# Kernel optimization log

Measured on AMD Instinct MI355X. Metric: run time of the kernel, lower is better.

Reference implementation:

```python
import jax, jax.numpy as jnp
import numpy as np

N_NODES = 40000      # batch of group nodes
DEGREE = 32          # neighbors (members) per node
NUM_USERS = 100000
NUM_GROUPS = 50000
EMBED_DIM = 64


def setup_inputs() -> dict:
    key = jax.random.key(0)
    ks = jax.random.split(key, 8)
    E = N_NODES * DEGREE
    d = EMBED_DIM
    return {
        "nodes": jax.random.randint(ks[0], (N_NODES,), 0, NUM_GROUPS),
        "neigh_idx": jax.random.randint(ks[1], (E,), 0, NUM_USERS),
        # edge i belongs to node segment_ids[i]; sorted, DEGREE edges per node
        "segment_ids": jnp.repeat(jnp.arange(N_NODES), DEGREE),
        "u2e_weight": jax.random.normal(ks[2], (NUM_USERS, d), jnp.float32) * 0.02,
        "g2e_weight": jax.random.normal(ks[3], (NUM_GROUPS, d), jnp.float32) * 0.02,
        "att1_w": jax.random.normal(ks[4], (d, 2 * d), jnp.float32) * (1.0 / np.sqrt(2 * d)),
        "att1_b": jnp.zeros((d,), jnp.float32),
        "att2_w": jax.random.normal(ks[5], (d, d), jnp.float32) * (1.0 / np.sqrt(d)),
        "att2_b": jnp.zeros((d,), jnp.float32),
        "att3_w": jax.random.normal(ks[6], (1, d), jnp.float32) * (1.0 / np.sqrt(d)),
        "att3_b": jnp.zeros((1,), jnp.float32),
    }


def _segment_softmax(logits, seg, num_segments):
    # numerically stable softmax within each node's neighbor segment
    m = jax.ops.segment_max(logits, seg, num_segments=num_segments)
    a = jnp.exp(logits - m[seg])
    s = jax.ops.segment_sum(a, seg, num_segments=num_segments)
    return a / s[seg]


def reference(nodes, neigh_idx, segment_ids, u2e_weight, g2e_weight,
              att1_w, att1_b, att2_w, att2_b, att3_w, att3_b):
    e_u = u2e_weight[neigh_idx]                 # [E, d] member embeddings
    g_rep = g2e_weight[nodes][segment_ids]      # [E, d] group query broadcast per edge
    x = jnp.concatenate([e_u, g_rep], axis=-1)  # [E, 2d]
    h = jax.nn.relu(x @ att1_w.T + att1_b)      # [E, d] (dropout inactive at eval)
    h = jax.nn.relu(h @ att2_w.T + att2_b)      # [E, d]
    logits = (h @ att3_w.T + att3_b)[:, 0]      # [E]
    att = _segment_softmax(logits, segment_ids, N_NODES)  # [E]
    # attention-weighted aggregation of member embeddings per node
    return jax.ops.segment_sum(att[:, None] * e_u, segment_ids, num_segments=N_NODES)  # [N, d]
```

## Files before the change

kernel.cpp:

```cpp
#include <hip/hip_runtime.h>
#include <hip/hip_bf16.h>

typedef __attribute__((ext_vector_type(8))) short short8;
typedef __attribute__((ext_vector_type(4))) float floatx4;

#define NNODES 40000
#define NPW 4
#define WAVES 8
#define NPB (NPW * WAVES)
#define NBLK (NNODES / NPB)

#define U2E_ELEMS (100000 * 64)
#define WS_ALIGN 256
#define WS_NEEDED ((size_t)U2E_ELEMS * 2 + WS_ALIGN)


__device__ __forceinline__ float bf2f(unsigned short s) {
    return __uint_as_float(((unsigned int)s) << 16);
}
__device__ __forceinline__ unsigned short f2bf(float f) {
    unsigned int u = __float_as_uint(f);
    u += 0x7fffu + ((u >> 16) & 1u);
    return (unsigned short)(u >> 16);
}
__device__ __forceinline__ unsigned short f2bf_fast(float f) {
#if __has_builtin(__builtin_amdgcn_cvt_pk_bf16_f32)
    auto r = __builtin_amdgcn_cvt_pk_bf16_f32(f, f);
    unsigned int u; __builtin_memcpy(&u, &r, 4);
    return (unsigned short)u;
#else
    return f2bf(f);
#endif
}
__device__ __forceinline__ short8 cvt8(const float* fp) {
    floatx4 a = *(const floatx4*)fp;
    floatx4 b = *(const floatx4*)(fp + 4);
    short8 r;
    #pragma unroll
    for (int j = 0; j < 4; ++j) {
        r[j]     = (short)f2bf_fast(a[j]);
        r[4 + j] = (short)f2bf_fast(b[j]);
    }
    return r;
}

__global__ __launch_bounds__(256) void convert_u2e(
    const float* __restrict__ u2e, unsigned short* __restrict__ ub) {
    const size_t i = ((size_t)blockIdx.x * 256 + threadIdx.x) * 8;
    if (i < U2E_ELEMS) *(short8*)(ub + i) = cvt8(u2e + i);
}

template<int PRE>
__global__ __launch_bounds__(512, 4) void gat_fused(
    const int*   __restrict__ nodes,
    const int*   __restrict__ neigh,
    const float* __restrict__ u2f,
    const unsigned short* __restrict__ u2b,
    const float* __restrict__ g2e,
    const float* __restrict__ w1,
    const float* __restrict__ b1,
    const float* __restrict__ w2,
    const float* __restrict__ b2,
    const float* __restrict__ w3,
    float* __restrict__ out)
{
    __shared__ alignas(16) short w1f[16 * 64 * 8];
    __shared__ alignas(16) short w2f[8 * 64 * 8];
    __shared__ alignas(16) short hbuf[WAVES][32 * 72];

    const int tid  = threadIdx.x;
    const int wv   = tid >> 6;
    const int lane = tid & 63;
    const int q    = lane >> 4;
    const int n16  = lane & 15;

    for (int i = tid; i < 16 * 64; i += 512) {
        int s = i >> 6, slot = i & 63;
        int nt = s >> 2, kc = s & 3;
        int row = nt * 16 + (slot & 15);
        int k   = kc * 32 + (slot >> 4) * 8;
        *(short8*)&w1f[i * 8] = cvt8(w1 + (size_t)row * 128 + k);
    }
    for (int i = tid; i < 8 * 64; i += 512) {
        int s = i >> 6, slot = i & 63;
        int nt = s >> 1, kc = s & 1;
        int row = nt * 16 + (slot & 15);
        int k   = kc * 32 + (slot >> 4) * 8;
        *(short8*)&w2f[i * 8] = cvt8(w2 + (size_t)row * 64 + k);
    }
    float b1v[4], b2v[4], w3v[4];
    #pragma unroll
    for (int nt = 0; nt < 4; ++nt) {
        b1v[nt] = b1[nt * 16 + n16];
        b2v[nt] = b2[nt * 16 + n16];
        w3v[nt] = w3[nt * 16 + n16];
    }
    __syncthreads();

    const int n0 = blockIdx.x * NPB + wv * NPW;

    int gc, vc, c0, c1;
    int gn, vn, d0, d1;
    short8 A00, A01, A10, A11, G0, G1;

    auto loadA = [&](int idx, int half) -> short8 {
        if (PRE) return *(const short8*)(u2b + (size_t)idx * 64 + half * 32 + q * 8);
        else     return cvt8(u2f + (size_t)idx * 64 + half * 32 + q * 8);
    };

    {
        gc = nodes[n0];
        size_t eb = (size_t)n0 * 32;
        vc = neigh[eb + (lane & 31)];
        c0 = neigh[eb + n16];
        c1 = neigh[eb + 16 + n16];
        A00 = loadA(c0, 0); A01 = loadA(c0, 1);
        A10 = loadA(c1, 0); A11 = loadA(c1, 1);
        G0  = cvt8(g2e + (size_t)gc * 64 + q * 8);
        G1  = cvt8(g2e + (size_t)gc * 64 + 32 + q * 8);
        int n1 = n0 + 1;
        gn = nodes[n1];
        size_t eb1 = (size_t)n1 * 32;
        vn = neigh[eb1 + (lane & 31)];
        d0 = neigh[eb1 + n16];
        d1 = neigh[eb1 + 16 + n16];
    }

    const floatx4 zero4 = {0.f, 0.f, 0.f, 0.f};

    for (int it = 0; it < NPW; ++it) {
        const int n = n0 + it;
        const short8 a00 = A00, a01 = A01, a10 = A10, a11 = A11, g0 = G0, g1 = G1;
        const int idxv = vc;

        floatx4 acc[2][4];
        #pragma unroll
        for (int mt = 0; mt < 2; ++mt)
            #pragma unroll
            for (int nt = 0; nt < 4; ++nt) acc[mt][nt] = zero4;
        #pragma unroll
        for (int kc = 0; kc < 4; ++kc) {
            short8 x0 = (kc == 0) ? a00 : (kc == 1) ? a01 : (kc == 2) ? g0 : g1;
            short8 x1 = (kc == 0) ? a10 : (kc == 1) ? a11 : (kc == 2) ? g0 : g1;
            #pragma unroll
            for (int nt = 0; nt < 4; ++nt) {
                short8 b = *(const short8*)&w1f[((nt * 4 + kc) * 64 + lane) * 8];
                acc[0][nt] = __builtin_amdgcn_mfma_f32_16x16x32_bf16(x0, b, acc[0][nt], 0, 0, 0);
                acc[1][nt] = __builtin_amdgcn_mfma_f32_16x16x32_bf16(x1, b, acc[1][nt], 0, 0, 0);
            }
        }

        if (it < NPW - 1) {
            A00 = loadA(d0, 0); A01 = loadA(d0, 1);
            A10 = loadA(d1, 0); A11 = loadA(d1, 1);
            G0  = cvt8(g2e + (size_t)gn * 64 + q * 8);
            G1  = cvt8(g2e + (size_t)gn * 64 + 32 + q * 8);
            gc = gn; vc = vn; c0 = d0; c1 = d1;
            int nn = n0 + it + 2; if (nn > NNODES - 1) nn = NNODES - 1;
            gn = nodes[nn];
            size_t eb2 = (size_t)nn * 32;
            vn = neigh[eb2 + (lane & 31)];
            d0 = neigh[eb2 + n16];
            d1 = neigh[eb2 + 16 + n16];
        }

        __builtin_amdgcn_wave_barrier();
        #pragma unroll
        for (int mt = 0; mt < 2; ++mt)
            #pragma unroll
            for (int nt = 0; nt < 4; ++nt)
                #pragma unroll
                for (int r = 0; r < 4; ++r) {
                    float v = fmaxf(acc[mt][nt][r] + b1v[nt], 0.f);
                    hbuf[wv][(mt * 16 + q * 4 + r) * 72 + nt * 16 + n16] = (short)f2bf_fast(v);
                }
        __builtin_amdgcn_wave_barrier();

        short8 a2[2][2];
        #pragma unroll
        for (int mt = 0; mt < 2; ++mt)
            #pragma unroll
            for (int kc = 0; kc < 2; ++kc)
                a2[mt][kc] = *(const short8*)&hbuf[wv][(mt * 16 + n16) * 72 + kc * 32 + q * 8];

        floatx4 acc2[2][4];
        #pragma unroll
        for (int mt = 0; mt < 2; ++mt)
            #pragma unroll
            for (int nt = 0; nt < 4; ++nt) acc2[mt][nt] = zero4;
        #pragma unroll
        for (int kc = 0; kc < 2; ++kc)
            #pragma unroll
            for (int nt = 0; nt < 4; ++nt) {
                short8 b = *(const short8*)&w2f[((nt * 2 + kc) * 64 + lane) * 8];
                acc2[0][nt] = __builtin_amdgcn_mfma_f32_16x16x32_bf16(a2[0][kc], b, acc2[0][nt], 0, 0, 0);
                acc2[1][nt] = __builtin_amdgcn_mfma_f32_16x16x32_bf16(a2[1][kc], b, acc2[1][nt], 0, 0, 0);
            }

        float tt[2][4];
        #pragma unroll
        for (int mt = 0; mt < 2; ++mt)
            #pragma unroll
            for (int r = 0; r < 4; ++r) {
                float s = 0.f;
                #pragma unroll
                for (int nt = 0; nt < 4; ++nt)
                    s = fmaf(fmaxf(acc2[mt][nt][r] + b2v[nt], 0.f), w3v[nt], s);
                s += __shfl_xor(s, 1, 64);
                s += __shfl_xor(s, 2, 64);
                s += __shfl_xor(s, 4, 64);
                s += __shfl_xor(s, 8, 64);
                tt[mt][r] = s;
            }
        const int j = n16 & 7;
        float v0 = (j & 2) ? ((j & 1) ? tt[0][3] : tt[0][2]) : ((j & 1) ? tt[0][1] : tt[0][0]);
        float v1 = (j & 2) ? ((j & 1) ? tt[1][3] : tt[1][2]) : ((j & 1) ? tt[1][1] : tt[1][0]);
        float vm = (j & 4) ? v1 : v0;
        const int m = lane & 31;
        const int src = ((m & 12) << 2) | (((m >> 4) & 1) << 2) | (m & 3);
        const float lg = __shfl(vm, src, 64);

        float mx = lg;
        #pragma unroll
        for (int off = 1; off < 32; off <<= 1)
            mx = fmaxf(mx, __shfl_xor(mx, off, 64));
        const float ex = __expf(lg - mx);
        float sm = ex;
        #pragma unroll
        for (int off = 1; off < 32; off <<= 1)
            sm += __shfl_xor(sm, off, 64);
        const float attv = ex / sm;

        float acco = 0.f;
        #pragma unroll 16
        for (int e2 = 0; e2 < 32; ++e2) {
            int   sidx = __builtin_amdgcn_readlane(idxv, e2);
            float a    = __uint_as_float(__builtin_amdgcn_readlane(__float_as_uint(attv), e2));
            float ev   = PRE ? bf2f(u2b[(size_t)sidx * 64 + lane])
                             : u2f[(size_t)sidx * 64 + lane];
            acco = fmaf(a, ev, acco);
        }
        out[(size_t)n * 64 + lane] = acco;
    }
}

extern "C" void kernel_launch(void* const* d_in, const int* in_sizes, int n_in,
                              void* d_out, int out_size, void* d_ws, size_t ws_size,
                              hipStream_t stream) {
    const int*   nodes = (const int*)d_in[0];
    const int*   neigh = (const int*)d_in[1];
    const float* u2e = (const float*)d_in[3];
    const float* g2e = (const float*)d_in[4];
    const float* w1  = (const float*)d_in[5];
    const float* b1  = (const float*)d_in[6];
    const float* w2  = (const float*)d_in[7];
    const float* b2  = (const float*)d_in[8];
    const float* w3  = (const float*)d_in[9];
    float* out = (float*)d_out;

    if (ws_size >= WS_NEEDED) {
        unsigned short* ub = (unsigned short*)(((uintptr_t)d_ws + WS_ALIGN - 1) & ~(uintptr_t)(WS_ALIGN - 1));
        hipLaunchKernelGGL(convert_u2e, dim3((U2E_ELEMS / 8 + 255) / 256), dim3(256),
                           0, stream, u2e, ub);
        hipLaunchKernelGGL(gat_fused<1>, dim3(NBLK), dim3(512), 0, stream,
                           nodes, neigh, u2e, ub, g2e, w1, b1, w2, b2, w3, out);
    } else {
        hipLaunchKernelGGL(gat_fused<0>, dim3(NBLK), dim3(512), 0, stream,
                           nodes, neigh, u2e, (const unsigned short*)nullptr,
                           g2e, w1, b1, w2, b2, w3, out);
    }
}
```

Baseline: 173.7 us.

## Keep layer-1 output in registers and reuse staged embeddings from LDS for aggregation

The MFMA operands are swapped so each layer computes the transposed product, and the weight rows are permuted so the layer-1 accumulators can be packed straight into layer-2 B operands, removing the hbuf LDS round trip. The member embeddings already held in registers are written to a swizzled per-wave LDS buffer, and the final weighted sum reads them from there instead of gathering u2e rows from global memory a second time. Bias and w3 vectors move to LDS, and the logit reduction becomes two cross-lane shuffles. The trade is extra LDS stores, plus a permuted layout whose index arithmetic must line up exactly with the MFMA fragment layout.

```diff
diff --git a/kernel.cpp b/kernel.cpp
--- a/kernel.cpp
+++ b/kernel.cpp
@@ -3,6 +3,7 @@
 
 typedef __attribute__((ext_vector_type(8))) short short8;
 typedef __attribute__((ext_vector_type(4))) float floatx4;
+typedef __attribute__((ext_vector_type(4))) unsigned int uintx4;
 
 #define NNODES 40000
 #define NPW 4
@@ -23,24 +24,26 @@
     u += 0x7fffu + ((u >> 16) & 1u);
     return (unsigned short)(u >> 16);
 }
-__device__ __forceinline__ unsigned short f2bf_fast(float f) {
+__device__ __forceinline__ unsigned int pk2bf(float lo, float hi) {
 #if __has_builtin(__builtin_amdgcn_cvt_pk_bf16_f32)
-    auto r = __builtin_amdgcn_cvt_pk_bf16_f32(f, f);
+    auto r = __builtin_amdgcn_cvt_pk_bf16_f32(lo, hi);
     unsigned int u; __builtin_memcpy(&u, &r, 4);
-    return (unsigned short)u;
+    return u;
 #else
-    return f2bf(f);
+    return (unsigned int)f2bf(lo) | ((unsigned int)f2bf(hi) << 16);
 #endif
 }
 __device__ __forceinline__ short8 cvt8(const float* fp) {
     floatx4 a = *(const floatx4*)fp;
     floatx4 b = *(const floatx4*)(fp + 4);
-    short8 r;
-    #pragma unroll
-    for (int j = 0; j < 4; ++j) {
-        r[j]     = (short)f2bf_fast(a[j]);
-        r[4 + j] = (short)f2bf_fast(b[j]);
-    }
+    uintx4 u;
+    u[0] = pk2bf(a[0], a[1]); u[1] = pk2bf(a[2], a[3]);
+    u[2] = pk2bf(b[0], b[1]); u[3] = pk2bf(b[2], b[3]);
+    short8 r; __builtin_memcpy(&r, &u, 16);
+    return r;
+}
+__device__ __forceinline__ short8 u4s8(uintx4 u) {
+    short8 r; __builtin_memcpy(&r, &u, 16);
     return r;
 }
 
@@ -48,6 +51,10 @@
     const float* __restrict__ u2e, unsigned short* __restrict__ ub) {
     const size_t i = ((size_t)blockIdx.x * 256 + threadIdx.x) * 8;
     if (i < U2E_ELEMS) *(short8*)(ub + i) = cvt8(u2e + i);
+}
+
+__device__ __forceinline__ int sigma_row(int dt, int m) {
+    return (dt & 1) * 32 + (m >> 2) * 8 + ((dt >> 1) << 2) + (m & 3);
 }
 
 template<int PRE>
@@ -66,7 +73,8 @@
 {
     __shared__ alignas(16) short w1f[16 * 64 * 8];
     __shared__ alignas(16) short w2f[8 * 64 * 8];
-    __shared__ alignas(16) short hbuf[WAVES][32 * 72];
+    __shared__ alignas(16) short ebuf[WAVES][2048];
+    __shared__ alignas(16) float bvec[192];
 
     const int tid  = threadIdx.x;
     const int wv   = tid >> 6;
@@ -76,31 +84,31 @@
 
     for (int i = tid; i < 16 * 64; i += 512) {
         int s = i >> 6, slot = i & 63;
-        int nt = s >> 2, kc = s & 3;
-        int row = nt * 16 + (slot & 15);
+        int dt = s >> 2, kc = s & 3;
+        int row = sigma_row(dt, slot & 15);
         int k   = kc * 32 + (slot >> 4) * 8;
         *(short8*)&w1f[i * 8] = cvt8(w1 + (size_t)row * 128 + k);
     }
     for (int i = tid; i < 8 * 64; i += 512) {
         int s = i >> 6, slot = i & 63;
-        int nt = s >> 1, kc = s & 1;
-        int row = nt * 16 + (slot & 15);
+        int ot = s >> 1, kc = s & 1;
+        int row = sigma_row(ot, slot & 15);
         int k   = kc * 32 + (slot >> 4) * 8;
         *(short8*)&w2f[i * 8] = cvt8(w2 + (size_t)row * 64 + k);
     }
-    float b1v[4], b2v[4], w3v[4];
+    for (int i = tid; i < 192; i += 512)
+        bvec[i] = (i < 64) ? b1[i] : (i < 128) ? b2[i - 64] : w3[i - 128];
+    __syncthreads();
+
+    const int n0 = blockIdx.x * NPB + wv * NPW;
+
+    const int ew0 = n16 * 64 + ((q ^ (n16 & 7)) * 8);
+    const int ew1 = n16 * 64 + (((4 + q) ^ (n16 & 7)) * 8);
+    int swz[8];
     #pragma unroll
-    for (int nt = 0; nt < 4; ++nt) {
-        b1v[nt] = b1[nt * 16 + n16];
-        b2v[nt] = b2[nt * 16 + n16];
-        w3v[nt] = w3[nt * 16 + n16];
-    }
-    __syncthreads();
-
-    const int n0 = blockIdx.x * NPB + wv * NPW;
-
-    int gc, vc, c0, c1;
-    int gn, vn, d0, d1;
+    for (int p = 0; p < 8; ++p) swz[p] = (((lane >> 3) ^ p) * 8) + (lane & 7);
+
+    int gn, d0, d1;
     short8 A00, A01, A10, A11, G0, G1;
 
     auto loadA = [&](int idx, int half) -> short8 {
@@ -109,116 +117,125 @@
     };
 
     {
-        gc = nodes[n0];
-        size_t eb = (size_t)n0 * 32;
-        vc = neigh[eb + (lane & 31)];
-        c0 = neigh[eb + n16];
-        c1 = neigh[eb + 16 + n16];
+        int g0i = nodes[n0];
+        size_t eb0 = (size_t)n0 * 32;
+        int c0 = neigh[eb0 + n16];
+        int c1 = neigh[eb0 + 16 + n16];
         A00 = loadA(c0, 0); A01 = loadA(c0, 1);
         A10 = loadA(c1, 0); A11 = loadA(c1, 1);
-        G0  = cvt8(g2e + (size_t)gc * 64 + q * 8);
-        G1  = cvt8(g2e + (size_t)gc * 64 + 32 + q * 8);
+        G0  = cvt8(g2e + (size_t)g0i * 64 + q * 8);
+        G1  = cvt8(g2e + (size_t)g0i * 64 + 32 + q * 8);
         int n1 = n0 + 1;
         gn = nodes[n1];
         size_t eb1 = (size_t)n1 * 32;
-        vn = neigh[eb1 + (lane & 31)];
         d0 = neigh[eb1 + n16];
         d1 = neigh[eb1 + 16 + n16];
     }
 
     const floatx4 zero4 = {0.f, 0.f, 0.f, 0.f};
+    int qo = q * 8;
 
     for (int it = 0; it < NPW; ++it) {
         const int n = n0 + it;
         const short8 a00 = A00, a01 = A01, a10 = A10, a11 = A11, g0 = G0, g1 = G1;
-        const int idxv = vc;
-
-        floatx4 acc[2][4];
-        #pragma unroll
-        for (int mt = 0; mt < 2; ++mt)
-            #pragma unroll
-            for (int nt = 0; nt < 4; ++nt) acc[mt][nt] = zero4;
+
+        floatx4 acc1[2][4];
+        #pragma unroll
+        for (int et = 0; et < 2; ++et)
+            #pragma unroll
+            for (int dt = 0; dt < 4; ++dt) acc1[et][dt] = zero4;
         #pragma unroll
         for (int kc = 0; kc < 4; ++kc) {
-            short8 x0 = (kc == 0) ? a00 : (kc == 1) ? a01 : (kc == 2) ? g0 : g1;
-            short8 x1 = (kc == 0) ? a10 : (kc == 1) ? a11 : (kc == 2) ? g0 : g1;
-            #pragma unroll
-            for (int nt = 0; nt < 4; ++nt) {
-                short8 b = *(const short8*)&w1f[((nt * 4 + kc) * 64 + lane) * 8];
-                acc[0][nt] = __builtin_amdgcn_mfma_f32_16x16x32_bf16(x0, b, acc[0][nt], 0, 0, 0);
-                acc[1][nt] = __builtin_amdgcn_mfma_f32_16x16x32_bf16(x1, b, acc[1][nt], 0, 0, 0);
-            }
+            const short8 x0 = (kc == 0) ? a00 : (kc == 1) ? a01 : (kc == 2) ? g0 : g1;
+            const short8 x1 = (kc == 0) ? a10 : (kc == 1) ? a11 : (kc == 2) ? g0 : g1;
+            #pragma unroll
+            for (int dt = 0; dt < 4; ++dt) {
+                const short8 w = *(const short8*)&w1f[((dt * 4 + kc) * 64 + lane) * 8];
+                acc1[0][dt] = __builtin_amdgcn_mfma_f32_16x16x32_bf16(w, x0, acc1[0][dt], 0, 0, 0);
+                acc1[1][dt] = __builtin_amdgcn_mfma_f32_16x16x32_bf16(w, x1, acc1[1][dt], 0, 0, 0);
+            }
+        }
+
+        {
+            short* ebw = &ebuf[wv][0];
+            *(short8*)&ebw[ew0]        = a00;
+            *(short8*)&ebw[ew1]        = a01;
+            *(short8*)&ebw[ew0 + 1024] = a10;
+            *(short8*)&ebw[ew1 + 1024] = a11;
         }
 
         if (it < NPW - 1) {
             A00 = loadA(d0, 0); A01 = loadA(d0, 1);
             A10 = loadA(d1, 0); A11 = loadA(d1, 1);
-            G0  = cvt8(g2e + (size_t)gn * 64 + q * 8);
-            G1  = cvt8(g2e + (size_t)gn * 64 + 32 + q * 8);
-            gc = gn; vc = vn; c0 = d0; c1 = d1;
+            G0  = cvt8(g2e + (size_t)gn * 64 + qo);
+            G1  = cvt8(g2e + (size_t)gn * 64 + 32 + qo);
             int nn = n0 + it + 2; if (nn > NNODES - 1) nn = NNODES - 1;
             gn = nodes[nn];
             size_t eb2 = (size_t)nn * 32;
-            vn = neigh[eb2 + (lane & 31)];
             d0 = neigh[eb2 + n16];
             d1 = neigh[eb2 + 16 + n16];
         }
 
-        __builtin_amdgcn_wave_barrier();
-        #pragma unroll
-        for (int mt = 0; mt < 2; ++mt)
-            #pragma unroll
-            for (int nt = 0; nt < 4; ++nt)
-                #pragma unroll
-                for (int r = 0; r < 4; ++r) {
-                    float v = fmaxf(acc[mt][nt][r] + b1v[nt], 0.f);
-                    hbuf[wv][(mt * 16 + q * 4 + r) * 72 + nt * 16 + n16] = (short)f2bf_fast(v);
-                }
-        __builtin_amdgcn_wave_barrier();
-
-        short8 a2[2][2];
-        #pragma unroll
-        for (int mt = 0; mt < 2; ++mt)
-            #pragma unroll
-            for (int kc = 0; kc < 2; ++kc)
-                a2[mt][kc] = *(const short8*)&hbuf[wv][(mt * 16 + n16) * 72 + kc * 32 + q * 8];
+        asm volatile("" : "+v"(qo));
+
+        floatx4 B1[2][2];
+        B1[0][0] = *(const floatx4*)&bvec[qo];
+        B1[0][1] = *(const floatx4*)&bvec[qo + 4];
+        B1[1][0] = *(const floatx4*)&bvec[qo + 32];
+        B1[1][1] = *(const floatx4*)&bvec[qo + 36];
+        short8 y[2][2];
+        #pragma unroll
+        for (int kc2 = 0; kc2 < 2; ++kc2)
+            #pragma unroll
+            for (int et = 0; et < 2; ++et) {
+                uintx4 u;
+                u[0] = pk2bf(fmaxf(acc1[et][kc2][0] + B1[kc2][0][0], 0.f),
+                             fmaxf(acc1[et][kc2][1] + B1[kc2][0][1], 0.f));
+                u[1] = pk2bf(fmaxf(acc1[et][kc2][2] + B1[kc2][0][2], 0.f),
+                             fmaxf(acc1[et][kc2][3] + B1[kc2][0][3], 0.f));
+                u[2] = pk2bf(fmaxf(acc1[et][kc2 + 2][0] + B1[kc2][1][0], 0.f),
+                             fmaxf(acc1[et][kc2 + 2][1] + B1[kc2][1][1], 0.f));
+                u[3] = pk2bf(fmaxf(acc1[et][kc2 + 2][2] + B1[kc2][1][2], 0.f),
+                             fmaxf(acc1[et][kc2 + 2][3] + B1[kc2][1][3], 0.f));
+                y[kc2][et] = u4s8(u);
+            }
 
         floatx4 acc2[2][4];
         #pragma unroll
-        for (int mt = 0; mt < 2; ++mt)
-            #pragma unroll
-            for (int nt = 0; nt < 4; ++nt) acc2[mt][nt] = zero4;
-        #pragma unroll
-        for (int kc = 0; kc < 2; ++kc)
-            #pragma unroll
-            for (int nt = 0; nt < 4; ++nt) {
-                short8 b = *(const short8*)&w2f[((nt * 2 + kc) * 64 + lane) * 8];
-                acc2[0][nt] = __builtin_amdgcn_mfma_f32_16x16x32_bf16(a2[0][kc], b, acc2[0][nt], 0, 0, 0);
-                acc2[1][nt] = __builtin_amdgcn_mfma_f32_16x16x32_bf16(a2[1][kc], b, acc2[1][nt], 0, 0, 0);
-            }
-
-        float tt[2][4];
-        #pragma unroll
-        for (int mt = 0; mt < 2; ++mt)
+        for (int et = 0; et < 2; ++et)
+            #pragma unroll
+            for (int ot = 0; ot < 4; ++ot) acc2[et][ot] = zero4;
+        #pragma unroll
+        for (int kc2 = 0; kc2 < 2; ++kc2)
+            #pragma unroll
+            for (int ot = 0; ot < 4; ++ot) {
+                const short8 w = *(const short8*)&w2f[((ot * 2 + kc2) * 64 + lane) * 8];
+                acc2[0][ot] = __builtin_amdgcn_mfma_f32_16x16x32_bf16(w, y[kc2][0], acc2[0][ot], 0, 0, 0);
+                acc2[1][ot] = __builtin_amdgcn_mfma_f32_16x16x32_bf16(w, y[kc2][1], acc2[1][ot], 0, 0, 0);
+            }
+
+        floatx4 B2[2][2], W3[2][2];
+        B2[0][0] = *(const floatx4*)&bvec[qo + 64];
+        B2[0][1] = *(const floatx4*)&bvec[qo + 68];
+        B2[1][0] = *(const floatx4*)&bvec[qo + 96];
+        B2[1][1] = *(const floatx4*)&bvec[qo + 100];
+        W3[0][0] = *(const floatx4*)&bvec[qo + 128];
+        W3[0][1] = *(const floatx4*)&bvec[qo + 132];
+        W3[1][0] = *(const floatx4*)&bvec[qo + 160];
+        W3[1][1] = *(const floatx4*)&bvec[qo + 164];
+        float s0 = 0.f, s1 = 0.f;
+        #pragma unroll
+        for (int ot = 0; ot < 4; ++ot) {
+            const int h = ot & 1, g = ot >> 1;
             #pragma unroll
             for (int r = 0; r < 4; ++r) {
-                float s = 0.f;
-                #pragma unroll
-                for (int nt = 0; nt < 4; ++nt)
-                    s = fmaf(fmaxf(acc2[mt][nt][r] + b2v[nt], 0.f), w3v[nt], s);
-                s += __shfl_xor(s, 1, 64);
-                s += __shfl_xor(s, 2, 64);
-                s += __shfl_xor(s, 4, 64);
-                s += __shfl_xor(s, 8, 64);
-                tt[mt][r] = s;
-            }
-        const int j = n16 & 7;
-        float v0 = (j & 2) ? ((j & 1) ? tt[0][3] : tt[0][2]) : ((j & 1) ? tt[0][1] : tt[0][0]);
-        float v1 = (j & 2) ? ((j & 1) ? tt[1][3] : tt[1][2]) : ((j & 1) ? tt[1][1] : tt[1][0]);
-        float vm = (j & 4) ? v1 : v0;
-        const int m = lane & 31;
-        const int src = ((m & 12) << 2) | (((m >> 4) & 1) << 2) | (m & 3);
-        const float lg = __shfl(vm, src, 64);
+                s0 = fmaf(fmaxf(acc2[0][ot][r] + B2[h][g][r], 0.f), W3[h][g][r], s0);
+                s1 = fmaf(fmaxf(acc2[1][ot][r] + B2[h][g][r], 0.f), W3[h][g][r], s1);
+            }
+        }
+        s0 += __shfl_xor(s0, 16, 64); s0 += __shfl_xor(s0, 32, 64);
+        s1 += __shfl_xor(s1, 16, 64); s1 += __shfl_xor(s1, 32, 64);
+        const float lg = ((lane >> 4) & 1) ? s1 : s0;
 
         float mx = lg;
         #pragma unroll
@@ -231,16 +248,17 @@
             sm += __shfl_xor(sm, off, 64);
         const float attv = ex / sm;
 
-        float acco = 0.f;
-        #pragma unroll 16
-        for (int e2 = 0; e2 < 32; ++e2) {
-            int   sidx = __builtin_amdgcn_readlane(idxv, e2);
-            float a    = __uint_as_float(__builtin_amdgcn_readlane(__float_as_uint(attv), e2));
-            float ev   = PRE ? bf2f(u2b[(size_t)sidx * 64 + lane])
-                             : u2f[(size_t)sidx * 64 + lane];
-            acco = fmaf(a, ev, acco);
-        }
-        out[(size_t)n * 64 + lane] = acco;
+        {
+            const short* ebw = &ebuf[wv][0];
+            float acco = 0.f;
+            #pragma unroll
+            for (int e = 0; e < 32; ++e) {
+                float a = __uint_as_float(__builtin_amdgcn_readlane(__float_as_uint(attv), e));
+                unsigned short ev = (unsigned short)ebw[e * 64 + swz[e & 7]];
+                acco = fmaf(a, bf2f(ev), acco);
+            }
+            out[(size_t)n * 64 + lane] = acco;
+        }
     }
 }
 
```

Result: faster. 157.7 us (-9.2%).
